# Performance work log

Measured on AMD Instinct MI355X. Metric: run time of the kernel, lower is better.

Reference implementation:

```python
import jax, jax.numpy as jnp
import numpy as np

N = 100_000      # nodes
E = 800_000      # edges (avg degree 8)
IN = 64          # in_channels
OUT = 64         # out_channels
HEADS = 4
HD = OUT // HEADS  # per-head out channels (concat=True)


def _unif(key, shape, fan_in):
    b = 1.0 / np.sqrt(fan_in)
    return jax.random.uniform(key, shape, jnp.float32, -b, b)


def setup_inputs() -> dict:
    key = jax.random.key(0)
    ks = jax.random.split(key, 12)
    x = jax.random.normal(ks[0], (N, IN), jnp.float32)
    pos = jax.random.normal(ks[1], (N, 3), jnp.float32)
    edge_index = jax.random.randint(ks[2], (2, E), 0, N, jnp.int32)
    # Per-head PointTransformerConv params (stacked over heads).
    # lin / lin_src / lin_dst are bias-free Linear(in, hd); pos_nn is Linear(3, hd) with bias.
    W_lin = _unif(ks[3], (HEADS, IN, HD), IN)
    W_src = _unif(ks[4], (HEADS, IN, HD), IN)
    W_dst = _unif(ks[5], (HEADS, IN, HD), IN)
    W_pos = _unif(ks[6], (HEADS, 3, HD), 3)
    b_pos = _unif(ks[7], (HEADS, HD), 3)
    # projection MLP: Linear(OUT,OUT) -> ReLU -> Linear(OUT,OUT)
    W1 = _unif(ks[8], (OUT, OUT), OUT)
    b1 = _unif(ks[9], (OUT,), OUT)
    W2 = _unif(ks[10], (OUT, OUT), OUT)
    b2 = _unif(ks[11], (OUT,), OUT)
    return dict(x=x, pos=pos, edge_index=edge_index, W_lin=W_lin, W_src=W_src,
                W_dst=W_dst, W_pos=W_pos, b_pos=b_pos, W1=W1, b1=b1, W2=W2, b2=b2)


def reference(x, pos, edge_index, W_lin, W_src, W_dst, W_pos, b_pos, W1, b1, W2, b2):
    # Add self-loops (PointTransformerConv default add_self_loops=True).
    loops = jnp.arange(N, dtype=edge_index.dtype)
    src = jnp.concatenate([edge_index[0], loops])   # j (source)
    dst = jnp.concatenate([edge_index[1], loops])   # i (target)

    # Per-node, all-heads projections: [N, H, HD]
    v = jnp.einsum('ni,hio->nho', x, W_lin)
    a_src = jnp.einsum('ni,hio->nho', x, W_src)
    a_dst = jnp.einsum('ni,hio->nho', x, W_dst)

    # Relative-position encoding delta = pos_nn(pos_i - pos_j): [Et, H, HD]
    rel = pos[dst] - pos[src]
    delta = jnp.einsum('ec,hco->eho', rel, W_pos) + b_pos

    # Attention logits per edge/channel: alpha_i - alpha_j + delta
    alpha = a_dst[dst] - a_src[src] + delta

    # Segment softmax over incoming edges of each target node (numerically stable).
    amax = jax.ops.segment_max(alpha, dst, num_segments=N)
    amax = jnp.where(jnp.isfinite(amax), amax, 0.0)
    ex = jnp.exp(alpha - amax[dst])
    denom = jax.ops.segment_sum(ex, dst, num_segments=N)
    attn = ex / jnp.maximum(denom[dst], 1e-16)

    # Message = attn * (lin(x_j) + delta), scatter-sum to targets: [N, H, HD]
    msg = attn * (v[src] + delta)
    out_h = jax.ops.segment_sum(msg, dst, num_segments=N)

    # Concat heads -> projection MLP
    out = out_h.reshape(N, HEADS * HD)
    h = jax.nn.relu(out @ W1 + b1)
    return h @ W2 + b2
```

## Files before the change

### kernel.cpp

```cpp
#include <hip/hip_runtime.h>
#include <math.h>


typedef _Float16 f16;
typedef _Float16 f16x2 __attribute__((ext_vector_type(2)));
typedef _Float16 f16x4 __attribute__((ext_vector_type(4)));
typedef _Float16 f16x8 __attribute__((ext_vector_type(8)));
typedef float f32x4 __attribute__((ext_vector_type(4)));

#define A_PITCH 104
#define C_PITCH 136
#define LOG2E 1.44269504f
#define S_CAP 32

__global__ __launch_bounds__(256) void zero_wprep_kernel(
    int Zb, int* __restrict__ cnt, int N,
    const float* __restrict__ Ws, const float* __restrict__ Wl,
    const float* __restrict__ Wp,
    const float* __restrict__ W1, const float* __restrict__ W2,
    f16* __restrict__ Bt, f16* __restrict__ W1p, f16* __restrict__ W2p)
{
    if ((int)blockIdx.x < Zb) {
        int i4 = (blockIdx.x * 256 + threadIdx.x) * 4;
        if (i4 + 3 < N) {
            *(int4*)&cnt[i4] = make_int4(0, 0, 0, 0);
        } else {
            for (int i = i4; i < N; i++) cnt[i] = 0;
        }
        return;
    }
    int idx = (blockIdx.x - Zb) * 256 + threadIdx.x;
    if (idx < 128 * 96) {
        int col = idx / 96, k = idx - col * 96;
        float v = 0.f;
        int p = col >> 1, h = p >> 4, o = p & 15;
        if (col & 1) {
            if (k < 64)      v = Wl[h * 1024 + k * 16 + o];
            else if (k < 67) v = -Wp[h * 48 + (k - 64) * 16 + o];
        } else {
            if (k < 64)      v = -LOG2E * Ws[h * 1024 + k * 16 + o];
            else if (k < 67) v = -LOG2E * Wp[h * 48 + (k - 64) * 16 + o];
        }
        Bt[col * 96 + k] = (f16)v;
    } else if (idx < 128 * 96 + 4096) {
        int t = idx - 128 * 96;
        int col = t >> 6, k = t & 63;
        W1p[col * 64 + k] = (f16)W1[k * 64 + col];
    } else if (idx < 128 * 96 + 8192) {
        int t = idx - 128 * 96 - 4096;
        int col = t >> 6, k = t & 63;
        W2p[col * 64 + k] = (f16)W2[k * 64 + col];
    }
}

__global__ __launch_bounds__(256) void gemm_hist_kernel(
    const float* __restrict__ x, const float* __restrict__ pos,
    const f16* __restrict__ Bt,
    f16* __restrict__ AV, int N, int Gb,
    const int* __restrict__ ei, int E, int Hb2,
    int* __restrict__ cnt, int* __restrict__ ssrc)
{
    __shared__ f16 smem[64 * C_PITCH];
    int tid = threadIdx.x;

    if (blockIdx.x & 1) {
        int hb = blockIdx.x >> 1;
        if (hb >= Hb2) return;
        int e0 = hb * 512 + tid;
        int e1 = e0 + 256;
        int s0 = 0, d0 = 0, s1 = 0, d1 = 0;
        bool a0 = e0 < E, a1 = e1 < E;
        if (a0) { s0 = ei[e0]; d0 = ei[E + e0]; }
        if (a1) { s1 = ei[e1]; d1 = ei[E + e1]; }
        if (a0) {
            int r = atomicAdd(&cnt[d0], 1);
            if (r < S_CAP) ssrc[d0 * S_CAP + r] = s0;
        }
        if (a1) {
            int r = atomicAdd(&cnt[d1], 1);
            if (r < S_CAP) ssrc[d1 * S_CAP + r] = s1;
        }
        return;
    }

    int gb = blockIdx.x >> 1;
    if (gb >= Gb) return;
    int l = tid & 63, wv = tid >> 6;
    int quad = l >> 4, lr = l & 15;
    int nb = gb * 64;

    for (int it = 0; it < 4; it++) {
        int q = it * 256 + tid;
        int n = q >> 4, k = (q & 15) * 4;
        float4 xv = make_float4(0.f, 0.f, 0.f, 0.f);
        if (nb + n < N) xv = *(const float4*)&x[(size_t)(nb + n) * 64 + k];
        f16x4 h4; h4[0] = (f16)xv.x; h4[1] = (f16)xv.y; h4[2] = (f16)xv.z; h4[3] = (f16)xv.w;
        *(f16x4*)&smem[n * A_PITCH + k] = h4;
    }
    {
        int n = tid >> 2, seg = tid & 3;
        f16x4 z = {(f16)0, (f16)0, (f16)0, (f16)0};
        f16x4 h4 = z;
        if (seg == 0 && nb + n < N) {
            h4[0] = (f16)pos[(size_t)(nb + n) * 3 + 0];
            h4[1] = (f16)pos[(size_t)(nb + n) * 3 + 1];
            h4[2] = (f16)pos[(size_t)(nb + n) * 3 + 2];
            h4[3] = (f16)1.0f;
        }
        *(f16x4*)&smem[n * A_PITCH + 64 + seg * 8] = h4;
        *(f16x4*)&smem[n * A_PITCH + 64 + seg * 8 + 4] = z;
    }
    __syncthreads();

    f16x8 af[4][3];
    #pragma unroll
    for (int mt = 0; mt < 4; mt++)
        #pragma unroll
        for (int kt = 0; kt < 3; kt++)
            af[mt][kt] = *(const f16x8*)&smem[(mt * 16 + lr) * A_PITCH + kt * 32 + quad * 8];
    __syncthreads();

    #pragma unroll
    for (int t = 0; t < 2; t++) {
        int colBase = (wv * 2 + t) * 16;
        f16x8 b0 = *(const f16x8*)&Bt[(colBase + lr) * 96 + 0  + quad * 8];
        f16x8 b1 = *(const f16x8*)&Bt[(colBase + lr) * 96 + 32 + quad * 8];
        f16x8 b2 = *(const f16x8*)&Bt[(colBase + lr) * 96 + 64 + quad * 8];
        #pragma unroll
        for (int mt = 0; mt < 4; mt++) {
            f32x4 acc = {0.f, 0.f, 0.f, 0.f};
            acc = __builtin_amdgcn_mfma_f32_16x16x32_f16(af[mt][0], b0, acc, 0, 0, 0);
            acc = __builtin_amdgcn_mfma_f32_16x16x32_f16(af[mt][1], b1, acc, 0, 0, 0);
            acc = __builtin_amdgcn_mfma_f32_16x16x32_f16(af[mt][2], b2, acc, 0, 0, 0);
            int col = colBase + lr;
            #pragma unroll
            for (int r = 0; r < 4; r++) {
                int row = mt * 16 + quad * 4 + r;
                smem[row * C_PITCH + col] = (f16)acc[r];
            }
        }
    }
    __syncthreads();

    for (int it = 0; it < 4; it++) {
        int cid = it * 256 + tid;
        int row = cid >> 4, off = (cid & 15) * 8;
        if (nb + row < N) {
            f16x8 w8 = *(const f16x8*)&smem[row * C_PITCH + off];
            f16x8 o;
            #pragma unroll
            for (int p = 0; p < 4; p++) {
                float e  = __builtin_amdgcn_exp2f((float)w8[2 * p]);
                float ev = e * (float)w8[2 * p + 1];
                o[2 * p]     = (f16)e;
                o[2 * p + 1] = (f16)ev;
            }
            *(f16x8*)&AV[(size_t)(nb + row) * 128 + off] = o;
        }
    }
}

__global__ __launch_bounds__(256) void attn_mlp_kernel(
    const f16* __restrict__ AV,
    const int* __restrict__ cnt, const int* __restrict__ ssrc,
    const float* __restrict__ pos, const float* __restrict__ Wp,
    const float* __restrict__ bp,
    const f16* __restrict__ W1p, const f16* __restrict__ W2p,
    const float* __restrict__ b1, const float* __restrict__ b2,
    float* __restrict__ out, int N)
{
    __shared__ f16 As[32 * 72];
    __shared__ f16 Hs[32 * 72];
    int tid = threadIdx.x, c = tid & 63, wv = tid >> 6;
    int quad = c >> 4, lr = c & 15;
    int nb = blockIdx.x * 32;

    float wpx = Wp[quad * 48 + 0  + lr];
    float wpy = Wp[quad * 48 + 16 + lr];
    float wpz = Wp[quad * 48 + 32 + lr];
    float bpc = bp[c];

    const f16x2* AV2 = (const f16x2*)AV;

    for (int pt = 0; pt < 4; pt++) {
        int i0 = __builtin_amdgcn_readfirstlane(nb + wv * 8 + pt * 2);
        int i1 = i0 + 1;
        if (i1 >= N) i1 = N - 1;
        if (i0 >= N) i0 = N - 1;
        int deg0 = __builtin_amdgcn_readfirstlane(cnt[i0]); if (deg0 > S_CAP) deg0 = S_CAP;
        int deg1 = __builtin_amdgcn_readfirstlane(cnt[i1]); if (deg1 > S_CAP) deg1 = S_CAP;
        float p0x = pos[i0 * 3 + 0], p0y = pos[i0 * 3 + 1], p0z = pos[i0 * 3 + 2];
        float p1x = pos[i1 * 3 + 0], p1y = pos[i1 * 3 + 1], p1z = pos[i1 * 3 + 2];
        f16x2 sv0 = AV2[(size_t)i0 * 64 + c];
        f16x2 sv1 = AV2[(size_t)i1 * 64 + c];
        float den0 = (float)sv0[0], num0 = (float)sv0[1];
        float den1 = (float)sv1[0], num1 = (float)sv1[1];
        int base0 = i0 * S_CAP, base1 = i1 * S_CAP;

        for (int b = 0; b < S_CAP; b += 8) {
            bool r0 = b < deg0, r1 = b < deg1;
            if (!(r0 | r1)) break;
            f16x2 w0[8], w1[8];
            if (r0) {
                #pragma unroll
                for (int s = 0; s < 8; s++) {
                    int jj = __builtin_amdgcn_readfirstlane(ssrc[base0 + b + s]);
                    if ((unsigned)jj >= (unsigned)N) jj = 0;
                    w0[s] = AV2[(size_t)jj * 64 + c];
                }
            }
            if (r1) {
                #pragma unroll
                for (int s = 0; s < 8; s++) {
                    int jj = __builtin_amdgcn_readfirstlane(ssrc[base1 + b + s]);
                    if ((unsigned)jj >= (unsigned)N) jj = 0;
                    w1[s] = AV2[(size_t)jj * 64 + c];
                }
            }
            if (r0) {
                #pragma unroll
                for (int s = 0; s < 8; s++) {
                    bool ok = (b + s) < deg0;
                    den0 += ok ? (float)w0[s][0] : 0.f;
                    num0 += ok ? (float)w0[s][1] : 0.f;
                }
            }
            if (r1) {
                #pragma unroll
                for (int s = 0; s < 8; s++) {
                    bool ok = (b + s) < deg1;
                    den1 += ok ? (float)w1[s][0] : 0.f;
                    num1 += ok ? (float)w1[s][1] : 0.f;
                }
            }
        }
        float Gi0 = p0x * wpx + p0y * wpy + p0z * wpz + bpc;
        float Gi1 = p1x * wpx + p1y * wpy + p1z * wpz + bpc;
        As[(wv * 8 + pt * 2) * 72 + c]     = (f16)(num0 / den0 + Gi0);
        As[(wv * 8 + pt * 2 + 1) * 72 + c] = (f16)(num1 / den1 + Gi1);
    }
    __syncthreads();

    f16x8 af[2][2];
    #pragma unroll
    for (int mt = 0; mt < 2; mt++)
        #pragma unroll
        for (int kt = 0; kt < 2; kt++)
            af[mt][kt] = *(const f16x8*)&As[(mt * 16 + lr) * 72 + kt * 32 + quad * 8];

    int col = wv * 16 + lr;
    f16x8 wb0 = *(const f16x8*)&W1p[col * 64 + quad * 8];
    f16x8 wb1 = *(const f16x8*)&W1p[col * 64 + 32 + quad * 8];
    float bias1 = b1[col];
    #pragma unroll
    for (int mt = 0; mt < 2; mt++) {
        f32x4 acc = {0.f, 0.f, 0.f, 0.f};
        acc = __builtin_amdgcn_mfma_f32_16x16x32_f16(af[mt][0], wb0, acc, 0, 0, 0);
        acc = __builtin_amdgcn_mfma_f32_16x16x32_f16(af[mt][1], wb1, acc, 0, 0, 0);
        #pragma unroll
        for (int r = 0; r < 4; r++) {
            int row = mt * 16 + quad * 4 + r;
            Hs[row * 72 + col] = (f16)fmaxf(acc[r] + bias1, 0.f);
        }
    }
    __syncthreads();

    f16x8 ag[2][2];
    #pragma unroll
    for (int mt = 0; mt < 2; mt++)
        #pragma unroll
        for (int kt = 0; kt < 2; kt++)
            ag[mt][kt] = *(const f16x8*)&Hs[(mt * 16 + lr) * 72 + kt * 32 + quad * 8];

    f16x8 wc0 = *(const f16x8*)&W2p[col * 64 + quad * 8];
    f16x8 wc1 = *(const f16x8*)&W2p[col * 64 + 32 + quad * 8];
    float bias2 = b2[col];
    #pragma unroll
    for (int mt = 0; mt < 2; mt++) {
        f32x4 acc = {0.f, 0.f, 0.f, 0.f};
        acc = __builtin_amdgcn_mfma_f32_16x16x32_f16(ag[mt][0], wc0, acc, 0, 0, 0);
        acc = __builtin_amdgcn_mfma_f32_16x16x32_f16(ag[mt][1], wc1, acc, 0, 0, 0);
        #pragma unroll
        for (int r = 0; r < 4; r++) {
            int row = nb + mt * 16 + quad * 4 + r;
            if (row < N) out[(size_t)row * 64 + col] = acc[r] + bias2;
        }
    }
}

extern "C" void kernel_launch(void* const* d_in, const int* in_sizes, int n_in,
                              void* d_out, int out_size, void* d_ws, size_t ws_size,
                              hipStream_t stream)
{
    const float* x    = (const float*)d_in[0];
    const float* pos  = (const float*)d_in[1];
    const int*   ei   = (const int*)d_in[2];
    const float* Wl   = (const float*)d_in[3];
    const float* Ws   = (const float*)d_in[4];
    const float* Wp   = (const float*)d_in[6];
    const float* bpos = (const float*)d_in[7];
    const float* W1   = (const float*)d_in[8];
    const float* b1   = (const float*)d_in[9];
    const float* W2   = (const float*)d_in[10];
    const float* b2   = (const float*)d_in[11];
    float* out = (float*)d_out;

    const int N = in_sizes[0] / 64;
    const int E = in_sizes[2] / 2;

    char* w = (char*)d_ws;
    f16*  AV   = (f16*)w;                   w += (size_t)N * 128 * 2;
    f16*  Bt   = (f16*)w;                   w += 128 * 96 * 2;
    f16*  W1p  = (f16*)w;                   w += 4096 * 2;
    f16*  W2p  = (f16*)w;                   w += 4096 * 2;
    int*  cnt  = (int*)w;                   w += (size_t)N * 4;
    int*  ssrc = (int*)w;                   w += (size_t)N * S_CAP * 4;

    const int Zb  = (N + 1023) / 1024;
    const int Pb  = (128 * 96 + 8192 + 255) / 256;
    const int Gb  = (N + 63) / 64;
    const int Hb2 = (E + 511) / 512;
    const int Kb  = (Gb > Hb2 ? Gb : Hb2) * 2;

    zero_wprep_kernel<<<Zb + Pb, 256, 0, stream>>>(Zb, cnt, N, Ws, Wl, Wp,
                                                   W1, W2, Bt, W1p, W2p);
    gemm_hist_kernel<<<Kb, 256, 0, stream>>>(x, pos, Bt, AV, N, Gb,
                                             ei, E, Hb2, cnt, ssrc);
    attn_mlp_kernel<<<(N + 31) / 32, 256, 0, stream>>>(AV, cnt, ssrc, pos, Wp, bpos,
                                                       W1p, W2p, b1, b2, out, N);
}
```

Measured before the change: 178.7 us.

## Bucket edges per 32-node block and build per-node lists in shared memory

Instead of per-node atomic counters and per-node global source lists, edges are scattered into per-32-node buckets. Each entry packs the source index and the local destination offset into one int. The attention kernel loads its bucket once, builds the per-node adjacency lists in LDS with shared atomics, then gathers from LDS. The aim is fewer global atomics and contiguous coalesced reads of the edge list, at the cost of an extra LDS pass and a bucket overflow cap (BCAP) that could drop edges for dense buckets. The packing also limits source indices to 17 bits.

```diff
diff --git a/kernel.cpp b/kernel.cpp
--- a/kernel.cpp
+++ b/kernel.cpp
@@ -12,9 +12,11 @@
 #define C_PITCH 136
 #define LOG2E 1.44269504f
 #define S_CAP 32
+#define BCAP 512
+#define SRC_MASK 131071
 
 __global__ __launch_bounds__(256) void zero_wprep_kernel(
-    int Zb, int* __restrict__ cnt, int N,
+    int Zb, int* __restrict__ cur, int NB,
     const float* __restrict__ Ws, const float* __restrict__ Wl,
     const float* __restrict__ Wp,
     const float* __restrict__ W1, const float* __restrict__ W2,
@@ -22,10 +24,10 @@
 {
     if ((int)blockIdx.x < Zb) {
         int i4 = (blockIdx.x * 256 + threadIdx.x) * 4;
-        if (i4 + 3 < N) {
-            *(int4*)&cnt[i4] = make_int4(0, 0, 0, 0);
+        if (i4 + 3 < NB) {
+            *(int4*)&cur[i4] = make_int4(0, 0, 0, 0);
         } else {
-            for (int i = i4; i < N; i++) cnt[i] = 0;
+            for (int i = i4; i < NB; i++) cur[i] = 0;
         }
         return;
     }
@@ -58,7 +60,7 @@
     const f16* __restrict__ Bt,
     f16* __restrict__ AV, int N, int Gb,
     const int* __restrict__ ei, int E, int Hb2,
-    int* __restrict__ cnt, int* __restrict__ ssrc)
+    int* __restrict__ cur, int* __restrict__ bk)
 {
     __shared__ f16 smem[64 * C_PITCH];
     int tid = threadIdx.x;
@@ -73,12 +75,14 @@
         if (a0) { s0 = ei[e0]; d0 = ei[E + e0]; }
         if (a1) { s1 = ei[e1]; d1 = ei[E + e1]; }
         if (a0) {
-            int r = atomicAdd(&cnt[d0], 1);
-            if (r < S_CAP) ssrc[d0 * S_CAP + r] = s0;
+            int bkt = d0 >> 5;
+            int r = atomicAdd(&cur[bkt], 1);
+            if (r < BCAP) bk[bkt * BCAP + r] = s0 | ((d0 & 31) << 17);
         }
         if (a1) {
-            int r = atomicAdd(&cnt[d1], 1);
-            if (r < S_CAP) ssrc[d1 * S_CAP + r] = s1;
+            int bkt = d1 >> 5;
+            int r = atomicAdd(&cur[bkt], 1);
+            if (r < BCAP) bk[bkt * BCAP + r] = s1 | ((d1 & 31) << 17);
         }
         return;
     }
@@ -162,7 +166,7 @@
 
 __global__ __launch_bounds__(256) void attn_mlp_kernel(
     const f16* __restrict__ AV,
-    const int* __restrict__ cnt, const int* __restrict__ ssrc,
+    const int* __restrict__ cur, const int* __restrict__ bk,
     const float* __restrict__ pos, const float* __restrict__ Wp,
     const float* __restrict__ bp,
     const f16* __restrict__ W1p, const f16* __restrict__ W2p,
@@ -171,9 +175,23 @@
 {
     __shared__ f16 As[32 * 72];
     __shared__ f16 Hs[32 * 72];
+    __shared__ int lst[32 * S_CAP];
+    __shared__ int ldeg[32];
     int tid = threadIdx.x, c = tid & 63, wv = tid >> 6;
     int quad = c >> 4, lr = c & 15;
-    int nb = blockIdx.x * 32;
+    int bkt = blockIdx.x;
+    int nb = bkt * 32;
+
+    if (tid < 32) ldeg[tid] = 0;
+    __syncthreads();
+    int cb = cur[bkt]; if (cb > BCAP) cb = BCAP;
+    for (int t = tid; t < cb; t += 256) {
+        int v = bk[bkt * BCAP + t];
+        int src = v & SRC_MASK, dl = (v >> 17) & 31;
+        int slot = atomicAdd(&ldeg[dl], 1);
+        if (slot < S_CAP) lst[dl * S_CAP + slot] = src;
+    }
+    __syncthreads();
 
     float wpx = Wp[quad * 48 + 0  + lr];
     float wpy = Wp[quad * 48 + 16 + lr];
@@ -183,41 +201,41 @@
     const f16x2* AV2 = (const f16x2*)AV;
 
     for (int pt = 0; pt < 4; pt++) {
-        int i0 = __builtin_amdgcn_readfirstlane(nb + wv * 8 + pt * 2);
+        int r0 = wv * 8 + pt * 2, r1 = r0 + 1;
+        int i0 = __builtin_amdgcn_readfirstlane(nb + r0);
         int i1 = i0 + 1;
         if (i1 >= N) i1 = N - 1;
         if (i0 >= N) i0 = N - 1;
-        int deg0 = __builtin_amdgcn_readfirstlane(cnt[i0]); if (deg0 > S_CAP) deg0 = S_CAP;
-        int deg1 = __builtin_amdgcn_readfirstlane(cnt[i1]); if (deg1 > S_CAP) deg1 = S_CAP;
+        int deg0 = __builtin_amdgcn_readfirstlane(ldeg[r0]); if (deg0 > S_CAP) deg0 = S_CAP;
+        int deg1 = __builtin_amdgcn_readfirstlane(ldeg[r1]); if (deg1 > S_CAP) deg1 = S_CAP;
         float p0x = pos[i0 * 3 + 0], p0y = pos[i0 * 3 + 1], p0z = pos[i0 * 3 + 2];
         float p1x = pos[i1 * 3 + 0], p1y = pos[i1 * 3 + 1], p1z = pos[i1 * 3 + 2];
         f16x2 sv0 = AV2[(size_t)i0 * 64 + c];
         f16x2 sv1 = AV2[(size_t)i1 * 64 + c];
         float den0 = (float)sv0[0], num0 = (float)sv0[1];
         float den1 = (float)sv1[0], num1 = (float)sv1[1];
-        int base0 = i0 * S_CAP, base1 = i1 * S_CAP;
 
         for (int b = 0; b < S_CAP; b += 8) {
-            bool r0 = b < deg0, r1 = b < deg1;
-            if (!(r0 | r1)) break;
+            bool g0 = b < deg0, g1 = b < deg1;
+            if (!(g0 | g1)) break;
             f16x2 w0[8], w1[8];
-            if (r0) {
+            if (g0) {
                 #pragma unroll
                 for (int s = 0; s < 8; s++) {
-                    int jj = __builtin_amdgcn_readfirstlane(ssrc[base0 + b + s]);
+                    int jj = __builtin_amdgcn_readfirstlane(lst[r0 * S_CAP + b + s]);
                     if ((unsigned)jj >= (unsigned)N) jj = 0;
                     w0[s] = AV2[(size_t)jj * 64 + c];
                 }
             }
-            if (r1) {
+            if (g1) {
                 #pragma unroll
                 for (int s = 0; s < 8; s++) {
-                    int jj = __builtin_amdgcn_readfirstlane(ssrc[base1 + b + s]);
+                    int jj = __builtin_amdgcn_readfirstlane(lst[r1 * S_CAP + b + s]);
                     if ((unsigned)jj >= (unsigned)N) jj = 0;
                     w1[s] = AV2[(size_t)jj * 64 + c];
                 }
             }
-            if (r0) {
+            if (g0) {
                 #pragma unroll
                 for (int s = 0; s < 8; s++) {
                     bool ok = (b + s) < deg0;
@@ -225,7 +243,7 @@
                     num0 += ok ? (float)w0[s][1] : 0.f;
                 }
             }
-            if (r1) {
+            if (g1) {
                 #pragma unroll
                 for (int s = 0; s < 8; s++) {
                     bool ok = (b + s) < deg1;
@@ -236,8 +254,8 @@
         }
         float Gi0 = p0x * wpx + p0y * wpy + p0z * wpz + bpc;
         float Gi1 = p1x * wpx + p1y * wpy + p1z * wpz + bpc;
-        As[(wv * 8 + pt * 2) * 72 + c]     = (f16)(num0 / den0 + Gi0);
-        As[(wv * 8 + pt * 2 + 1) * 72 + c] = (f16)(num1 / den1 + Gi1);
+        As[r0 * 72 + c] = (f16)(num0 / den0 + Gi0);
+        As[r1 * 72 + c] = (f16)(num1 / den1 + Gi1);
     }
     __syncthreads();
 
@@ -307,25 +325,26 @@
 
     const int N = in_sizes[0] / 64;
     const int E = in_sizes[2] / 2;
+    const int NB = (N + 31) / 32;
 
     char* w = (char*)d_ws;
     f16*  AV   = (f16*)w;                   w += (size_t)N * 128 * 2;
     f16*  Bt   = (f16*)w;                   w += 128 * 96 * 2;
     f16*  W1p  = (f16*)w;                   w += 4096 * 2;
     f16*  W2p  = (f16*)w;                   w += 4096 * 2;
-    int*  cnt  = (int*)w;                   w += (size_t)N * 4;
-    int*  ssrc = (int*)w;                   w += (size_t)N * S_CAP * 4;
-
-    const int Zb  = (N + 1023) / 1024;
+    int*  cur  = (int*)w;                   w += (size_t)NB * 4;
+    int*  bk   = (int*)w;                   w += (size_t)NB * BCAP * 4;
+
+    const int Zb  = (NB + 1023) / 1024;
     const int Pb  = (128 * 96 + 8192 + 255) / 256;
     const int Gb  = (N + 63) / 64;
     const int Hb2 = (E + 511) / 512;
     const int Kb  = (Gb > Hb2 ? Gb : Hb2) * 2;
 
-    zero_wprep_kernel<<<Zb + Pb, 256, 0, stream>>>(Zb, cnt, N, Ws, Wl, Wp,
+    zero_wprep_kernel<<<Zb + Pb, 256, 0, stream>>>(Zb, cur, NB, Ws, Wl, Wp,
                                                    W1, W2, Bt, W1p, W2p);
     gemm_hist_kernel<<<Kb, 256, 0, stream>>>(x, pos, Bt, AV, N, Gb,
-                                             ei, E, Hb2, cnt, ssrc);
-    attn_mlp_kernel<<<(N + 31) / 32, 256, 0, stream>>>(AV, cnt, ssrc, pos, Wp, bpos,
-                                                       W1p, W2p, b1, b2, out, N);
+                                             ei, E, Hb2, cur, bk);
+    attn_mlp_kernel<<<NB, 256, 0, stream>>>(AV, cur, bk, pos, Wp, bpos,
+                                            W1p, W2p, b1, b2, out, N);
 }
```

Result: slower. 211.0 us (+18.1%).
